# Optimization experiments

Hardware: AMD Instinct MI355X
Metric: run time of the kernel (lower is better)

## Reference

```python
import jax, jax.numpy as jnp
import numpy as np

T = 2048
D_IN = 1024
D_OUT = 1024
N_HEAD = 16
HEAD_DIM = D_OUT // N_HEAD


def setup_inputs() -> dict:
    key = jax.random.key(0)
    kx, kq, kk, kv = jax.random.split(key, 4)
    s = 1.0 / np.sqrt(D_IN)
    return {
        "x": jax.random.normal(kx, (T, D_IN), dtype=jnp.float32),
        "W_q": jax.random.normal(kq, (D_OUT, D_IN), dtype=jnp.float32) * s,
        "W_k": jax.random.normal(kk, (D_OUT, D_IN), dtype=jnp.float32) * s,
        "W_v": jax.random.normal(kv, (D_OUT, D_IN), dtype=jnp.float32) * s,
    }


def reference(x, W_q, W_k, W_v):
    t = x.shape[0]
    # linear projections (torch Linear: y = x @ W.T), split into heads: [H, T, Dh]
    q = (x @ W_q.T).reshape(t, N_HEAD, HEAD_DIM).transpose(1, 0, 2)
    k = (x @ W_k.T).reshape(t, N_HEAD, HEAD_DIM).transpose(1, 0, 2)
    v = (x @ W_v.T).reshape(t, N_HEAD, HEAD_DIM).transpose(1, 0, 2)
    # raw scores [H, T, T]
    omega = jnp.einsum("hqd,hkd->hqk", q, k)
    causal = jnp.triu(jnp.ones((t, t), dtype=bool), k=1)
    omega = jnp.where(causal[None, :, :], -jnp.inf, omega)
    # NOTE: faithful to source quirk — divides by head_dim**(-0.5),
    # i.e. multiplies scores by sqrt(head_dim)
    att_w = jax.nn.softmax(omega * (HEAD_DIM ** 0.5), axis=-1)
    context = jnp.einsum("hqk,hkd->hqd", att_w, v)  # [H, T, Dh]
    return context.transpose(1, 0, 2).reshape(t, D_OUT)
```

## Files before the change

kernel.cpp:

```cpp
#include <hip/hip_runtime.h>
#include <hip/hip_bf16.h>


typedef __bf16 bf16x8 __attribute__((ext_vector_type(8)));
typedef __bf16 bf16x4 __attribute__((ext_vector_type(4)));
typedef __bf16 bf16x2 __attribute__((ext_vector_type(2)));
typedef float  f32x4  __attribute__((ext_vector_type(4)));

#define MFMA(a, b, c) __builtin_amdgcn_mfma_f32_16x16x32_bf16((a), (b), (c), 0, 0, 0)

#if __has_builtin(__builtin_amdgcn_exp2f)
#define EXP2F(x) __builtin_amdgcn_exp2f(x)
#else
#define EXP2F(x) exp2f(x)
#endif

constexpr int T = 2048, DIN = 1024, DOUT = 1024, NH = 16, DH = 64;
constexpr float SC = 11.5415603f;
constexpr float DEFER = 0.6931472f;

constexpr size_t SZ_XMAT = (size_t)T * DIN * 2;
constexpr size_t SZ_WMAT = (size_t)DOUT * DIN * 2;
constexpr size_t OFF_XH = 0;
constexpr size_t OFF_XL = OFF_XH + SZ_XMAT;
constexpr size_t OFF_QH = OFF_XL + SZ_XMAT;
constexpr size_t OFF_QL = OFF_QH + SZ_XMAT;
constexpr size_t OFF_KH = OFF_QL + SZ_XMAT;
constexpr size_t OFF_KL = OFF_KH + SZ_XMAT;
constexpr size_t OFF_VT = OFF_KL + SZ_XMAT;
constexpr size_t OFF_W  = OFF_VT + SZ_XMAT;

__device__ __forceinline__ void gload_lds16(const void* g, void* l) {
  __builtin_amdgcn_global_load_lds(
      (const __attribute__((address_space(1))) void*)g,
      (__attribute__((address_space(3))) void*)l, 16, 0, 0);
}

__global__ void split_all(const float* __restrict__ x, const float* __restrict__ wq,
                          const float* __restrict__ wk, const float* __restrict__ wv,
                          char* __restrict__ ws) {
  const int i = blockIdx.x * 256 + threadIdx.x;
  const float* src;
  __bf16 *hi, *lo;
  int off;
  if (i < T * DIN / 4) {
    src = x; off = i;
    hi = (__bf16*)(ws + OFF_XH);
    lo = (__bf16*)(ws + OFF_XL);
  } else {
    const int j = i - T * DIN / 4;
    const int z = j >> 18;
    off = j & 262143;
    src = (z == 0) ? wq : ((z == 1) ? wk : wv);
    hi = (__bf16*)(ws + OFF_W + (size_t)z * 2 * SZ_WMAT);
    lo = hi + (size_t)DOUT * DIN;
  }
  const f32x4 v = ((const f32x4*)src)[off];
  bf16x4 h, l;
#pragma unroll
  for (int j = 0; j < 4; ++j) {
    const float xv = v[j];
    const __bf16 hh = (__bf16)xv;
    h[j] = hh;
    l[j] = (__bf16)(xv - (float)hh);
  }
  ((bf16x4*)hi)[off] = h;
  ((bf16x4*)lo)[off] = l;
}

template <bool SPLIT>
__device__ __forceinline__ void proj_loop(const __bf16* __restrict__ Ah,
                                          const __bf16* __restrict__ Al,
                                          const __bf16* __restrict__ Bh,
                                          const __bf16* __restrict__ Bl,
                                          __bf16* lds, int tm, int tn, int lane,
                                          int wv, f32x4 (&acc)[4][4]) {
  constexpr int BUF = SPLIT ? 16384 : 8192;
  constexpr int BOFF = SPLIT ? 8192 : 4096;
  const int wm = wv >> 1, wn = wv & 1;
  const int q4 = lane >> 4, r16 = lane & 15;

  auto STAGE = [&](int ks, int buf) {
    const int k0 = ks * 32;
    __bf16* base = lds + buf * BUF;
#pragma unroll
    for (int j = 0; j < 2; ++j) {
      const int cbase = wv * 128 + j * 64;
      const int cidx = cbase + lane;
      const int row = cidx & 127, kc = cidx >> 7;
      const size_t ga = (size_t)(tm + row) * DIN + k0 + kc * 8;
      const size_t gb = (size_t)(tn + row) * DIN + k0 + kc * 8;
      gload_lds16(Ah + ga, base + cbase * 8);
      gload_lds16(Bh + gb, base + BOFF + cbase * 8);
      if constexpr (SPLIT) {
        gload_lds16(Al + ga, base + 4096 + cbase * 8);
        gload_lds16(Bl + gb, base + 12288 + cbase * 8);
      }
    }
  };

  STAGE(0, 0);
  STAGE(1, 1);

  for (int ks = 0; ks < 32; ++ks) {
    const int buf = ks & 1;
    if (ks < 31) {
      if constexpr (SPLIT) asm volatile("s_waitcnt vmcnt(8)" ::: "memory");
      else                 asm volatile("s_waitcnt vmcnt(4)" ::: "memory");
    } else {
      asm volatile("s_waitcnt vmcnt(0)" ::: "memory");
    }
    __builtin_amdgcn_s_barrier();
    __builtin_amdgcn_sched_barrier(0);

    const __bf16* ldsA = lds + buf * BUF;
    const __bf16* ldsB = ldsA + BOFF;

    bf16x8 fah[4], fbh[4], fal[4], fbl[4];
#pragma unroll
    for (int b = 0; b < 4; ++b) {
      const int ra = wm * 64 + b * 16 + r16;
      const int rb = wn * 64 + b * 16 + r16;
      fah[b] = *(const bf16x8*)(ldsA + (q4 * 128 + ra) * 8);
      fbh[b] = *(const bf16x8*)(ldsB + (q4 * 128 + rb) * 8);
      if constexpr (SPLIT) {
        fal[b] = *(const bf16x8*)(ldsA + 4096 + (q4 * 128 + ra) * 8);
        fbl[b] = *(const bf16x8*)(ldsB + 4096 + (q4 * 128 + rb) * 8);
      }
    }
    __builtin_amdgcn_s_setprio(1);
#pragma unroll
    for (int bm = 0; bm < 4; ++bm)
#pragma unroll
      for (int bn = 0; bn < 4; ++bn) {
        acc[bm][bn] = MFMA(fah[bm], fbh[bn], acc[bm][bn]);
        if constexpr (SPLIT) {
          acc[bm][bn] = MFMA(fah[bm], fbl[bn], acc[bm][bn]);
          acc[bm][bn] = MFMA(fal[bm], fbh[bn], acc[bm][bn]);
        }
      }
    __builtin_amdgcn_s_setprio(0);
    asm volatile("s_waitcnt lgkmcnt(0)" ::: "memory");
    __builtin_amdgcn_sched_barrier(0);
    __builtin_amdgcn_s_barrier();
    __builtin_amdgcn_sched_barrier(0);
    if (ks < 30) STAGE(ks + 2, buf);
  }
}

__global__ __launch_bounds__(256, 2) void qkv_proj(char* ws) {
  const int bid = blockIdx.x;
  const int z = bid >> 7;
  const int t_ = bid & 127;
  const int tm = (t_ >> 3) * 128;
  const int tn = (t_ & 7) * 128;
  const int tid = threadIdx.x;
  const int lane = tid & 63, wv = tid >> 6;
  const int wm = wv >> 1, wn = wv & 1;
  const int q4 = lane >> 4, r16 = lane & 15;

  const __bf16* Ah = (const __bf16*)(ws + OFF_XH);
  const __bf16* Al = (const __bf16*)(ws + OFF_XL);
  const __bf16* Bh = (const __bf16*)(ws + OFF_W + (size_t)z * 2 * SZ_WMAT);
  const __bf16* Bl = Bh + (size_t)DOUT * DIN;

  __shared__ alignas(16) __bf16 lds[32768];

  f32x4 acc[4][4] = {};

  if (z < 2) {
    proj_loop<true>(Ah, Al, Bh, Bl, lds, tm, tn, lane, wv, acc);
    __bf16* Oh = (__bf16*)(ws + (z == 0 ? OFF_QH : OFF_KH));
    __bf16* Ol = (__bf16*)(ws + (z == 0 ? OFF_QL : OFF_KL));
#pragma unroll
    for (int bm = 0; bm < 4; ++bm)
#pragma unroll
      for (int bn = 0; bn < 4; ++bn)
#pragma unroll
        for (int r = 0; r < 4; ++r) {
          const int t = tm + wm * 64 + bm * 16 + q4 * 4 + r;
          const int n = tn + wn * 64 + bn * 16 + r16;
          const float v = acc[bm][bn][r];
          const __bf16 hh = (__bf16)v;
          Oh[(size_t)t * DOUT + n] = hh;
          Ol[(size_t)t * DOUT + n] = (__bf16)(v - (float)hh);
        }
  } else {
    proj_loop<false>(Ah, Al, Bh, Bl, lds, tm, tn, lane, wv, acc);
    __syncthreads();
    __bf16* tb = lds;
#pragma unroll
    for (int bm = 0; bm < 4; ++bm)
#pragma unroll
      for (int bn = 0; bn < 4; ++bn)
#pragma unroll
        for (int r = 0; r < 4; ++r) {
          const int tl = wm * 64 + bm * 16 + q4 * 4 + r;
          const int nl = wn * 64 + bn * 16 + r16;
          tb[(size_t)nl * 136 + tl] = (__bf16)acc[bm][bn][r];
        }
    __syncthreads();
    __bf16* Vt = (__bf16*)(ws + OFF_VT);
#pragma unroll
    for (int it = 0; it < 8; ++it) {
      const int cid = it * 256 + tid;
      const int nl = cid >> 4, tc = cid & 15;
      const bf16x8 vd = *(const bf16x8*)(tb + (size_t)nl * 136 + tc * 8);
      *(bf16x8*)(Vt + (size_t)(tn + nl) * T + tm + tc * 8) = vd;
    }
  }
}

__global__ __launch_bounds__(256, 2) void attn_kernel(const char* __restrict__ ws,
                                                      float* __restrict__ out) {
  const int bid = blockIdx.x;
  const int h = bid & 15;
  const int qt = (bid < 256) ? (31 - (bid >> 4)) : ((bid - 256) >> 4);
  const int tid = threadIdx.x;
  const int lane = tid & 63, wid = tid >> 6;
  const int q4 = lane >> 4, r16 = lane & 15;

  const __bf16* Qh = (const __bf16*)(ws + OFF_QH);
  const __bf16* Ql = (const __bf16*)(ws + OFF_QL);
  const __bf16* Kh = (const __bf16*)(ws + OFF_KH);
  const __bf16* Kl = (const __bf16*)(ws + OFF_KL);
  const __bf16* Vt = (const __bf16*)(ws + OFF_VT);

  __shared__ alignas(16) __bf16 sKh[2][64 * 72];
  __shared__ alignas(16) __bf16 sKl[2][64 * 72];
  __shared__ alignas(16) __bf16 sVt[2][64 * 72];
  __shared__ alignas(16) __bf16 sP[4][16 * 72];

  const int qbase = qt * 64 + wid * 16;
  const int qg = qbase + r16;

  bf16x8 fqh[2], fql[2];
#pragma unroll
  for (int c = 0; c < 2; ++c) {
    const size_t off = (size_t)qg * DOUT + h * 64 + c * 32 + q4 * 8;
    fqh[c] = *(const bf16x8*)(Qh + off);
    fql[c] = *(const bf16x8*)(Ql + off);
  }

  bf16x8 st[6];
  const int srow0 = tid >> 3, sdc = tid & 7;
  const int srow1 = 32 + srow0;
  auto ISSUE = [&](int kvt) {
    const int kv0 = kvt * 64;
    const size_t k0 = (size_t)(kv0 + srow0) * DOUT + h * 64 + sdc * 8;
    const size_t k1 = (size_t)(kv0 + srow1) * DOUT + h * 64 + sdc * 8;
    st[0] = *(const bf16x8*)(Kh + k0);
    st[1] = *(const bf16x8*)(Kl + k0);
    st[2] = *(const bf16x8*)(Vt + (size_t)(h * 64 + srow0) * T + kv0 + sdc * 8);
    st[3] = *(const bf16x8*)(Kh + k1);
    st[4] = *(const bf16x8*)(Kl + k1);
    st[5] = *(const bf16x8*)(Vt + (size_t)(h * 64 + srow1) * T + kv0 + sdc * 8);
  };
  auto WRITE = [&](int b) {
    *(bf16x8*)(&sKh[b][srow0 * 72 + sdc * 8]) = st[0];
    *(bf16x8*)(&sKl[b][srow0 * 72 + sdc * 8]) = st[1];
    *(bf16x8*)(&sVt[b][srow0 * 72 + sdc * 8]) = st[2];
    *(bf16x8*)(&sKh[b][srow1 * 72 + sdc * 8]) = st[3];
    *(bf16x8*)(&sKl[b][srow1 * 72 + sdc * 8]) = st[4];
    *(bf16x8*)(&sVt[b][srow1 * 72 + sdc * 8]) = st[5];
  };

  f32x4 accT[4] = {};
  float mrun = -1e30f, lrun = 0.f;

  ISSUE(0);
  asm volatile("s_waitcnt vmcnt(0)" ::: "memory");
  WRITE(0);
  if (qt > 0) ISSUE(1);
  asm volatile("s_waitcnt lgkmcnt(0)" ::: "memory");
  __builtin_amdgcn_s_barrier();
  __builtin_amdgcn_sched_barrier(0);

  for (int kvt = 0; kvt <= qt; ++kvt) {
    const int cur = kvt & 1;
    const int kv0 = kvt * 64;
    const int nb = (kvt == qt) ? (wid + 1) : 4;
    f32x4 s[4];
    __builtin_amdgcn_s_setprio(1);
#pragma unroll
    for (int blk = 0; blk < 4; ++blk) {
      if (blk < nb) {
        f32x4 a = {};
#pragma unroll
        for (int c = 0; c < 2; ++c) {
          const int ko = (blk * 16 + r16) * 72 + c * 32 + q4 * 8;
          const bf16x8 kh = *(const bf16x8*)(&sKh[cur][ko]);
          const bf16x8 kl = *(const bf16x8*)(&sKl[cur][ko]);
          a = MFMA(kh, fqh[c], a);
          a = MFMA(kl, fqh[c], a);
          a = MFMA(kh, fql[c], a);
        }
        s[blk] = a;
      } else {
        s[blk] = f32x4{-1e30f, -1e30f, -1e30f, -1e30f};
      }
    }
    __builtin_amdgcn_s_setprio(0);

    if (kvt == qt) {
#pragma unroll
      for (int blk = 0; blk < 4; ++blk)
#pragma unroll
        for (int r = 0; r < 4; ++r) {
          const int k = kv0 + blk * 16 + q4 * 4 + r;
          if (k > qg) s[blk][r] = -1e30f;
        }
    }

    const float m0 = fmaxf(fmaxf(s[0][0], s[0][1]), fmaxf(s[0][2], s[0][3]));
    const float m1 = fmaxf(fmaxf(s[1][0], s[1][1]), fmaxf(s[1][2], s[1][3]));
    const float m2 = fmaxf(fmaxf(s[2][0], s[2][1]), fmaxf(s[2][2], s[2][3]));
    const float m3 = fmaxf(fmaxf(s[3][0], s[3][1]), fmaxf(s[3][2], s[3][3]));
    float mx = fmaxf(fmaxf(m0, m1), fmaxf(m2, m3));
    mx = fmaxf(mx, __shfl_xor(mx, 16, 64));
    mx = fmaxf(mx, __shfl_xor(mx, 32, 64));

    if (__any(mx - mrun > DEFER)) {
      const float mnew = fmaxf(mrun, mx);
      const float scale = EXP2F((mrun - mnew) * SC);
      mrun = mnew;
      lrun *= scale;
#pragma unroll
      for (int d = 0; d < 4; ++d) accT[d] *= scale;
    }
    const float mn2 = mrun * SC;

    float ps = 0.f;
#pragma unroll
    for (int blk = 0; blk < 4; ++blk)
#pragma unroll
      for (int rp = 0; rp < 2; ++rp) {
        const float p0 = EXP2F(__builtin_fmaf(s[blk][2 * rp], SC, -mn2));
        const float p1 = EXP2F(__builtin_fmaf(s[blk][2 * rp + 1], SC, -mn2));
        ps += p0 + p1;
        bf16x2 w;
        w[0] = (__bf16)p0;
        w[1] = (__bf16)p1;
        *(bf16x2*)(&sP[wid][r16 * 72 + blk * 16 + q4 * 4 + 2 * rp]) = w;
      }
    ps += __shfl_xor(ps, 16, 64);
    ps += __shfl_xor(ps, 32, 64);
    lrun += ps;

    asm volatile("s_waitcnt lgkmcnt(0)" ::: "memory");
    __builtin_amdgcn_sched_barrier(0);

    __builtin_amdgcn_s_setprio(1);
#pragma unroll
    for (int c = 0; c < 2; ++c) {
      const bf16x8 pb = *(const bf16x8*)(&sP[wid][r16 * 72 + c * 32 + q4 * 8]);
#pragma unroll
      for (int d = 0; d < 4; ++d) {
        const bf16x8 va =
            *(const bf16x8*)(&sVt[cur][(d * 16 + r16) * 72 + c * 32 + q4 * 8]);
        accT[d] = MFMA(va, pb, accT[d]);
      }
    }
    __builtin_amdgcn_s_setprio(0);

    if (kvt < qt) {
      asm volatile("s_waitcnt vmcnt(0)" ::: "memory");
      WRITE(cur ^ 1);
      if (kvt + 1 < qt) ISSUE(kvt + 2);
    }
    asm volatile("s_waitcnt lgkmcnt(0)" ::: "memory");
    __builtin_amdgcn_sched_barrier(0);
    __builtin_amdgcn_s_barrier();
    __builtin_amdgcn_sched_barrier(0);
  }

  const float rl = 1.0f / lrun;
#pragma unroll
  for (int d = 0; d < 4; ++d)
#pragma unroll
    for (int r = 0; r < 4; ++r)
      out[(size_t)qg * DOUT + h * 64 + d * 16 + q4 * 4 + r] = accT[d][r] * rl;
}

extern "C" void kernel_launch(void* const* d_in, const int* in_sizes, int n_in,
                              void* d_out, int out_size, void* d_ws, size_t ws_size,
                              hipStream_t stream) {
  const float* x  = (const float*)d_in[0];
  const float* Wq = (const float*)d_in[1];
  const float* Wk = (const float*)d_in[2];
  const float* Wv = (const float*)d_in[3];
  char* ws = (char*)d_ws;

  split_all<<<5120, 256, 0, stream>>>(x, Wq, Wk, Wv, ws);
  qkv_proj<<<384, 256, 0, stream>>>(ws);
  attn_kernel<<<512, 256, 0, stream>>>(ws, (float*)d_out);
}
```

Measured before the change: 102.5 us.

## Switch attention to 32x32x16 MFMA with register-resident P via lane shuffles

The attention kernel now uses 2 waves per block (128 threads), each owning 32 query rows, and computes scores and PV with 32x32x16 bf16 MFMAs instead of 16x16x32. The softmax probabilities stay in registers and are rearranged into the B-operand layout with cross-half lane shuffles, so the sP shared-memory round trip is gone. The goal is fewer LDS reads per MFMA and no P staging. The cost is fewer waves per block, each loading more K/V staging registers, plus more accumulator registers, which may lower occupancy or reduce latency hiding.

Result: slower. 118.8 us (+16.0%).

```diff
diff --git a/kernel.cpp b/kernel.cpp
--- a/kernel.cpp
+++ b/kernel.cpp
@@ -4,10 +4,14 @@
 
 typedef __bf16 bf16x8 __attribute__((ext_vector_type(8)));
 typedef __bf16 bf16x4 __attribute__((ext_vector_type(4)));
-typedef __bf16 bf16x2 __attribute__((ext_vector_type(2)));
 typedef float  f32x4  __attribute__((ext_vector_type(4)));
+typedef float  f32x16 __attribute__((ext_vector_type(16)));
+typedef unsigned int u32;
+typedef u32 u32x2 __attribute__((ext_vector_type(2)));
+typedef u32 u32x4 __attribute__((ext_vector_type(4)));
 
 #define MFMA(a, b, c) __builtin_amdgcn_mfma_f32_16x16x32_bf16((a), (b), (c), 0, 0, 0)
+#define MFMA32(a, b, c) __builtin_amdgcn_mfma_f32_32x32x16_bf16((a), (b), (c), 0, 0, 0)
 
 #if __has_builtin(__builtin_amdgcn_exp2f)
 #define EXP2F(x) __builtin_amdgcn_exp2f(x)
@@ -211,14 +215,15 @@
   }
 }
 
-__global__ __launch_bounds__(256, 2) void attn_kernel(const char* __restrict__ ws,
+__global__ __launch_bounds__(128, 2) void attn_kernel(const char* __restrict__ ws,
                                                       float* __restrict__ out) {
   const int bid = blockIdx.x;
   const int h = bid & 15;
   const int qt = (bid < 256) ? (31 - (bid >> 4)) : ((bid - 256) >> 4);
   const int tid = threadIdx.x;
   const int lane = tid & 63, wid = tid >> 6;
-  const int q4 = lane >> 4, r16 = lane & 15;
+  const int r32 = lane & 31, hi = lane >> 5;
+  const int hi8 = hi * 8;
 
   const __bf16* Qh = (const __bf16*)(ws + OFF_QH);
   const __bf16* Ql = (const __bf16*)(ws + OFF_QL);
@@ -229,43 +234,42 @@
   __shared__ alignas(16) __bf16 sKh[2][64 * 72];
   __shared__ alignas(16) __bf16 sKl[2][64 * 72];
   __shared__ alignas(16) __bf16 sVt[2][64 * 72];
-  __shared__ alignas(16) __bf16 sP[4][16 * 72];
-
-  const int qbase = qt * 64 + wid * 16;
-  const int qg = qbase + r16;
-
-  bf16x8 fqh[2], fql[2];
-#pragma unroll
-  for (int c = 0; c < 2; ++c) {
-    const size_t off = (size_t)qg * DOUT + h * 64 + c * 32 + q4 * 8;
-    fqh[c] = *(const bf16x8*)(Qh + off);
-    fql[c] = *(const bf16x8*)(Ql + off);
-  }
-
-  bf16x8 st[6];
-  const int srow0 = tid >> 3, sdc = tid & 7;
-  const int srow1 = 32 + srow0;
+
+  const int qbase = qt * 64 + wid * 32;
+  const int qg = qbase + r32;
+
+  bf16x8 fqh[4], fql[4];
+#pragma unroll
+  for (int ds = 0; ds < 4; ++ds) {
+    const size_t off = (size_t)qg * DOUT + h * 64 + ds * 16 + hi8;
+    fqh[ds] = *(const bf16x8*)(Qh + off);
+    fql[ds] = *(const bf16x8*)(Ql + off);
+  }
+
+  bf16x8 st[12];
+  const int srow = tid >> 3, sdc = tid & 7;
   auto ISSUE = [&](int kvt) {
     const int kv0 = kvt * 64;
-    const size_t k0 = (size_t)(kv0 + srow0) * DOUT + h * 64 + sdc * 8;
-    const size_t k1 = (size_t)(kv0 + srow1) * DOUT + h * 64 + sdc * 8;
-    st[0] = *(const bf16x8*)(Kh + k0);
-    st[1] = *(const bf16x8*)(Kl + k0);
-    st[2] = *(const bf16x8*)(Vt + (size_t)(h * 64 + srow0) * T + kv0 + sdc * 8);
-    st[3] = *(const bf16x8*)(Kh + k1);
-    st[4] = *(const bf16x8*)(Kl + k1);
-    st[5] = *(const bf16x8*)(Vt + (size_t)(h * 64 + srow1) * T + kv0 + sdc * 8);
+#pragma unroll
+    for (int k = 0; k < 4; ++k) {
+      const int row = srow + 16 * k;
+      const size_t koff = (size_t)(kv0 + row) * DOUT + h * 64 + sdc * 8;
+      st[3 * k + 0] = *(const bf16x8*)(Kh + koff);
+      st[3 * k + 1] = *(const bf16x8*)(Kl + koff);
+      st[3 * k + 2] = *(const bf16x8*)(Vt + (size_t)(h * 64 + row) * T + kv0 + sdc * 8);
+    }
   };
   auto WRITE = [&](int b) {
-    *(bf16x8*)(&sKh[b][srow0 * 72 + sdc * 8]) = st[0];
-    *(bf16x8*)(&sKl[b][srow0 * 72 + sdc * 8]) = st[1];
-    *(bf16x8*)(&sVt[b][srow0 * 72 + sdc * 8]) = st[2];
-    *(bf16x8*)(&sKh[b][srow1 * 72 + sdc * 8]) = st[3];
-    *(bf16x8*)(&sKl[b][srow1 * 72 + sdc * 8]) = st[4];
-    *(bf16x8*)(&sVt[b][srow1 * 72 + sdc * 8]) = st[5];
+#pragma unroll
+    for (int k = 0; k < 4; ++k) {
+      const int row = srow + 16 * k;
+      *(bf16x8*)(&sKh[b][row * 72 + sdc * 8]) = st[3 * k + 0];
+      *(bf16x8*)(&sKl[b][row * 72 + sdc * 8]) = st[3 * k + 1];
+      *(bf16x8*)(&sVt[b][row * 72 + sdc * 8]) = st[3 * k + 2];
+    }
   };
 
-  f32x4 accT[4] = {};
+  f32x16 acc0 = {}, acc1 = {};
   float mrun = -1e30f, lrun = 0.f;
 
   ISSUE(0);
@@ -279,45 +283,48 @@
   for (int kvt = 0; kvt <= qt; ++kvt) {
     const int cur = kvt & 1;
     const int kv0 = kvt * 64;
-    const int nb = (kvt == qt) ? (wid + 1) : 4;
-    f32x4 s[4];
+    const bool diag = (kvt == qt);
+
+    f32x16 s0 = {}, s1 = {};
+    const bool do1 = !(diag && wid == 0);
     __builtin_amdgcn_s_setprio(1);
 #pragma unroll
-    for (int blk = 0; blk < 4; ++blk) {
-      if (blk < nb) {
-        f32x4 a = {};
-#pragma unroll
-        for (int c = 0; c < 2; ++c) {
-          const int ko = (blk * 16 + r16) * 72 + c * 32 + q4 * 8;
-          const bf16x8 kh = *(const bf16x8*)(&sKh[cur][ko]);
-          const bf16x8 kl = *(const bf16x8*)(&sKl[cur][ko]);
-          a = MFMA(kh, fqh[c], a);
-          a = MFMA(kl, fqh[c], a);
-          a = MFMA(kh, fql[c], a);
-        }
-        s[blk] = a;
-      } else {
-        s[blk] = f32x4{-1e30f, -1e30f, -1e30f, -1e30f};
+    for (int ds = 0; ds < 4; ++ds) {
+      const int ko = ds * 16 + hi8;
+      const bf16x8 kh0 = *(const bf16x8*)(&sKh[cur][r32 * 72 + ko]);
+      const bf16x8 kl0 = *(const bf16x8*)(&sKl[cur][r32 * 72 + ko]);
+      s0 = MFMA32(kh0, fqh[ds], s0);
+      s0 = MFMA32(kl0, fqh[ds], s0);
+      s0 = MFMA32(kh0, fql[ds], s0);
+    }
+    if (do1) {
+#pragma unroll
+      for (int ds = 0; ds < 4; ++ds) {
+        const int ko = ds * 16 + hi8;
+        const bf16x8 kh1 = *(const bf16x8*)(&sKh[cur][(32 + r32) * 72 + ko]);
+        const bf16x8 kl1 = *(const bf16x8*)(&sKl[cur][(32 + r32) * 72 + ko]);
+        s1 = MFMA32(kh1, fqh[ds], s1);
+        s1 = MFMA32(kl1, fqh[ds], s1);
+        s1 = MFMA32(kh1, fql[ds], s1);
       }
     }
     __builtin_amdgcn_s_setprio(0);
 
-    if (kvt == qt) {
-#pragma unroll
-      for (int blk = 0; blk < 4; ++blk)
-#pragma unroll
-        for (int r = 0; r < 4; ++r) {
-          const int k = kv0 + blk * 16 + q4 * 4 + r;
-          if (k > qg) s[blk][r] = -1e30f;
-        }
-    }
-
-    const float m0 = fmaxf(fmaxf(s[0][0], s[0][1]), fmaxf(s[0][2], s[0][3]));
-    const float m1 = fmaxf(fmaxf(s[1][0], s[1][1]), fmaxf(s[1][2], s[1][3]));
-    const float m2 = fmaxf(fmaxf(s[2][0], s[2][1]), fmaxf(s[2][2], s[2][3]));
-    const float m3 = fmaxf(fmaxf(s[3][0], s[3][1]), fmaxf(s[3][2], s[3][3]));
-    float mx = fmaxf(fmaxf(m0, m1), fmaxf(m2, m3));
-    mx = fmaxf(mx, __shfl_xor(mx, 16, 64));
+    if (diag) {
+#pragma unroll
+      for (int r = 0; r < 16; ++r) {
+        const int kr = (r & 3) + 8 * (r >> 2) + 4 * hi;
+        if (kv0 + kr > qg) s0[r] = -1e30f;
+        if (kv0 + 32 + kr > qg) s1[r] = -1e30f;
+      }
+    }
+
+    float mx = -1e30f;
+#pragma unroll
+    for (int r = 0; r < 16; ++r) {
+      mx = fmaxf(mx, s0[r]);
+      mx = fmaxf(mx, s1[r]);
+    }
     mx = fmaxf(mx, __shfl_xor(mx, 32, 64));
 
     if (__any(mx - mrun > DEFER)) {
@@ -326,40 +333,56 @@
       mrun = mnew;
       lrun *= scale;
 #pragma unroll
-      for (int d = 0; d < 4; ++d) accT[d] *= scale;
+      for (int r = 0; r < 16; ++r) {
+        acc0[r] *= scale;
+        acc1[r] *= scale;
+      }
     }
     const float mn2 = mrun * SC;
 
     float ps = 0.f;
 #pragma unroll
-    for (int blk = 0; blk < 4; ++blk)
-#pragma unroll
-      for (int rp = 0; rp < 2; ++rp) {
-        const float p0 = EXP2F(__builtin_fmaf(s[blk][2 * rp], SC, -mn2));
-        const float p1 = EXP2F(__builtin_fmaf(s[blk][2 * rp + 1], SC, -mn2));
-        ps += p0 + p1;
-        bf16x2 w;
-        w[0] = (__bf16)p0;
-        w[1] = (__bf16)p1;
-        *(bf16x2*)(&sP[wid][r16 * 72 + blk * 16 + q4 * 4 + 2 * rp]) = w;
-      }
-    ps += __shfl_xor(ps, 16, 64);
+    for (int r = 0; r < 16; ++r) {
+      s0[r] = EXP2F(__builtin_fmaf(s0[r], SC, -mn2));
+      s1[r] = EXP2F(__builtin_fmaf(s1[r], SC, -mn2));
+      ps += s0[r] + s1[r];
+    }
     ps += __shfl_xor(ps, 32, 64);
     lrun += ps;
 
-    asm volatile("s_waitcnt lgkmcnt(0)" ::: "memory");
-    __builtin_amdgcn_sched_barrier(0);
+    bf16x8 pb[4];
+#pragma unroll
+    for (int ks = 0; ks < 4; ++ks) {
+      const int rb = (ks & 1) * 8;
+      bf16x4 lo4, hi4;
+#pragma unroll
+      for (int j = 0; j < 4; ++j) {
+        const float pl = (ks < 2) ? s0[rb + j] : s1[rb + j];
+        const float ph = (ks < 2) ? s0[rb + 4 + j] : s1[rb + 4 + j];
+        lo4[j] = (__bf16)pl;
+        hi4[j] = (__bf16)ph;
+      }
+      const u32x2 L = __builtin_bit_cast(u32x2, lo4);
+      const u32x2 H = __builtin_bit_cast(u32x2, hi4);
+      u32x4 f;
+#pragma unroll
+      for (int t = 0; t < 2; ++t) {
+        const u32 send = hi ? L[t] : H[t];
+        const u32 recv = (u32)__shfl_xor((int)send, 32, 64);
+        f[t] = hi ? recv : L[t];
+        f[2 + t] = hi ? H[t] : recv;
+      }
+      pb[ks] = __builtin_bit_cast(bf16x8, f);
+    }
 
     __builtin_amdgcn_s_setprio(1);
 #pragma unroll
-    for (int c = 0; c < 2; ++c) {
-      const bf16x8 pb = *(const bf16x8*)(&sP[wid][r16 * 72 + c * 32 + q4 * 8]);
-#pragma unroll
-      for (int d = 0; d < 4; ++d) {
-        const bf16x8 va =
-            *(const bf16x8*)(&sVt[cur][(d * 16 + r16) * 72 + c * 32 + q4 * 8]);
-        accT[d] = MFMA(va, pb, accT[d]);
-      }
+    for (int ks = 0; ks < 4; ++ks) {
+      const int vo = ks * 16 + hi8;
+      const bf16x8 va0 = *(const bf16x8*)(&sVt[cur][r32 * 72 + vo]);
+      const bf16x8 va1 = *(const bf16x8*)(&sVt[cur][(32 + r32) * 72 + vo]);
+      acc0 = MFMA32(va0, pb[ks], acc0);
+      acc1 = MFMA32(va1, pb[ks], acc1);
     }
     __builtin_amdgcn_s_setprio(0);
 
@@ -376,10 +399,11 @@
 
   const float rl = 1.0f / lrun;
 #pragma unroll
-  for (int d = 0; d < 4; ++d)
-#pragma unroll
-    for (int r = 0; r < 4; ++r)
-      out[(size_t)qg * DOUT + h * 64 + d * 16 + q4 * 4 + r] = accT[d][r] * rl;
+  for (int r = 0; r < 16; ++r) {
+    const int d = (r & 3) + 8 * (r >> 2) + 4 * hi;
+    out[(size_t)qg * DOUT + h * 64 + d] = acc0[r] * rl;
+    out[(size_t)qg * DOUT + h * 64 + 32 + d] = acc1[r] * rl;
+  }
 }
 
 extern "C" void kernel_launch(void* const* d_in, const int* in_sizes, int n_in,
@@ -393,5 +417,5 @@
 
   split_all<<<5120, 256, 0, stream>>>(x, Wq, Wk, Wv, ws);
   qkv_proj<<<384, 256, 0, stream>>>(ws);
-  attn_kernel<<<512, 256, 0, stream>>>(ws, (float*)d_out);
-}
+  attn_kernel<<<512, 128, 0, stream>>>(ws, (float*)d_out);
+}
```
